# Performance work log

Hardware: AMD Instinct MI355X
Metric: run time of the kernel (lower is better)

## Reference

```python
import jax, jax.numpy as jnp
import numpy as np

ALPHA = 0.5  # distance-decay base (self.alpha)

def setup_inputs() -> dict:
    key = jax.random.key(0)
    N, E, D_IN, D_OUT = 50000, 800000, 128, 128
    k1, k2, k3, k4, k5 = jax.random.split(key, 5)
    h = jax.random.normal(k1, (N, D_IN), dtype=jnp.float32)
    # first N edges are self-loops so every node has in/out degree >= 1
    src = jnp.concatenate([jnp.arange(N), jax.random.randint(k2, (E - N,), 0, N)]).astype(jnp.int32)
    dst = jnp.concatenate([jnp.arange(N), jax.random.randint(k3, (E - N,), 0, N)]).astype(jnp.int32)
    distance = jax.random.randint(k4, (E,), 0, 6).astype(jnp.int32)
    limit = float(np.sqrt(6.0 / (D_IN + D_OUT)))  # xavier_uniform
    weight = jax.random.uniform(k5, (D_IN, D_OUT), jnp.float32, -limit, limit)
    bias = jnp.zeros((D_OUT,), jnp.float32)
    return {"h": h, "src": src, "dst": dst, "distance": distance, "weight": weight, "bias": bias}

def reference(h, src, dst, distance, weight, bias):
    N = h.shape[0]
    ones = jnp.ones(src.shape[0], jnp.float32)
    out_deg = jax.ops.segment_sum(ones, src, num_segments=N)  # [N]
    in_deg = jax.ops.segment_sum(ones, dst, num_segments=N)   # [N]
    # source-side symmetric norm
    feat = h * (out_deg ** -0.5)[:, None]                     # [N, D]
    # per-edge message: gathered src feature * alpha^distance
    w = jnp.power(jnp.float32(ALPHA), distance.astype(jnp.float32))  # [E]
    msg = feat[src] * w[:, None]                              # [E, D]
    # mean over mailbox == segment-sum / in-degree
    agg = jax.ops.segment_sum(msg, dst, num_segments=N) / in_deg[:, None]  # [N, D]
    rst = agg @ weight                                        # [N, D_OUT]
    rst = rst * (in_deg ** -0.5)[:, None] + bias
    return rst
```

## Files before the change

kernel.cpp:

```cpp
#include <hip/hip_runtime.h>


constexpr int D = 128;
constexpr int HC = 32;
constexpr int NWMAX = 25088;
constexpr int PNODES = 32;
constexpr int PCAP = 768;
constexpr int CHUNK = 8192;

typedef __attribute__((ext_vector_type(8))) short bf16x8;
typedef __attribute__((ext_vector_type(4))) float f32x4;

__device__ __forceinline__ float bf16_to_f(unsigned int u16) {
    union { unsigned int u; float f; } c; c.u = u16 << 16; return c.f;
}
__device__ __forceinline__ unsigned int f_to_bf16(float f) {
    union { float f; unsigned int u; } c; c.f = f;
    unsigned int u = c.u;
    u += 0x7fffu + ((u >> 16) & 1u);
    return u >> 16;
}

__global__ __launch_bounds__(256) void k_hist(const int* __restrict__ key,
        unsigned int* __restrict__ slices, int E, int NW, int chunk) {
    __shared__ unsigned int bins[NWMAX];
    for (int i = threadIdx.x; i < NW; i += 256) bins[i] = 0;
    __syncthreads();
    int c = blockIdx.x;
    int e0 = c * chunk, e1 = min(e0 + chunk, E);
    for (int i = e0 + threadIdx.x * 4; i < e1; i += 1024) {
        if (i + 3 < e1) {
            int4 k4 = *(const int4*)&key[i];
            atomicAdd(&bins[k4.x >> 1], 1u << ((k4.x & 1) * 16));
            atomicAdd(&bins[k4.y >> 1], 1u << ((k4.y & 1) * 16));
            atomicAdd(&bins[k4.z >> 1], 1u << ((k4.z & 1) * 16));
            atomicAdd(&bins[k4.w >> 1], 1u << ((k4.w & 1) * 16));
        } else {
            for (int e = i; e < e1; e++)
                atomicAdd(&bins[key[e] >> 1], 1u << ((key[e] & 1) * 16));
        }
    }
    __syncthreads();
    unsigned int* o = slices + (size_t)c * NW;
    for (int i = threadIdx.x; i < NW; i += 256) o[i] = bins[i];
}

__global__ __launch_bounds__(256) void k_scale_cast(const unsigned int* __restrict__ slices,
        const float4* __restrict__ h4, uint4* __restrict__ hs4,
        const float* __restrict__ W, unsigned short* __restrict__ Wt,
        int N, int NW, int wblk) {
    if (blockIdx.x == wblk) {
        for (int i = threadIdx.x; i < D * D; i += 256) {
            int k = i >> 7, n = i & 127;
            Wt[n * D + k] = (unsigned short)f_to_bf16(W[i]);
        }
        return;
    }
    __shared__ float osc[256];
    int n0 = blockIdx.x * 256;
    int n = n0 + threadIdx.x;
    if (n < N) {
        int wi = n >> 1, sh = (n & 1) * 16;
        unsigned int s = 0;
        #pragma unroll 8
        for (int c = 0; c < HC; c++) s += slices[(size_t)c * NW + wi];
        osc[threadIdx.x] = rsqrtf((float)((s >> sh) & 0xffffu));
    }
    __syncthreads();
    int grp = threadIdx.x >> 4, lane = threadIdx.x & 15;
    int rend = min(256, N - n0);
    for (int r = grp; r < rend; r += 16) {
        int row = n0 + r;
        float sc = osc[r];
        float4 a = h4[(size_t)row * 32 + lane * 2];
        float4 b = h4[(size_t)row * 32 + lane * 2 + 1];
        uint4 o;
        o.x = f_to_bf16(a.x * sc) | (f_to_bf16(a.y * sc) << 16);
        o.y = f_to_bf16(a.z * sc) | (f_to_bf16(a.w * sc) << 16);
        o.z = f_to_bf16(b.x * sc) | (f_to_bf16(b.y * sc) << 16);
        o.w = f_to_bf16(b.z * sc) | (f_to_bf16(b.w * sc) << 16);
        hs4[(size_t)row * 16 + lane] = o;
    }
}

__global__ __launch_bounds__(256) void k_partition(const int* __restrict__ src,
        const int* __restrict__ dst, const int* __restrict__ dist,
        int* __restrict__ gcur, unsigned int* __restrict__ gbuf, int E, int P) {
    __shared__ unsigned int sorted[CHUNK];
    __shared__ int gidx[CHUNK];
    extern __shared__ int dyn[];
    int* hist = dyn;
    int* start = dyn + P;
    int* lofs = dyn + 2 * P;
    int* base_g = dyn + 3 * P;
    __shared__ int wsum[4];

    int tid = threadIdx.x;
    int lane = tid & 63, w = tid >> 6;
    int e0 = blockIdx.x * CHUNK;
    int e1 = min(e0 + CHUNK, E);
    int ce = e1 - e0;

    for (int b = tid; b < P; b += 256) hist[b] = 0;
    __syncthreads();

    for (int i = e0 + tid * 4; i < e1; i += 1024) {
        if (i + 3 < e1) {
            int4 d4 = *(const int4*)&dst[i];
            atomicAdd(&hist[d4.x >> 5], 1);
            atomicAdd(&hist[d4.y >> 5], 1);
            atomicAdd(&hist[d4.z >> 5], 1);
            atomicAdd(&hist[d4.w >> 5], 1);
        } else {
            for (int e = i; e < e1; e++) atomicAdd(&hist[dst[e] >> 5], 1);
        }
    }
    __syncthreads();

    int loc[7];
    int s = 0;
    #pragma unroll
    for (int j = 0; j < 7; j++) {
        int b = tid * 7 + j;
        int v = (b < P) ? hist[b] : 0;
        loc[j] = s;
        s += v;
    }
    int x = s;
    #pragma unroll
    for (int off = 1; off < 64; off <<= 1) {
        int t = __shfl_up(x, off, 64);
        if (lane >= off) x += t;
    }
    if (lane == 63) wsum[w] = x;
    __syncthreads();
    int tbase = x - s;
    #pragma unroll
    for (int k = 0; k < 4; k++) if (k < w) tbase += wsum[k];
    #pragma unroll
    for (int j = 0; j < 7; j++) {
        int b = tid * 7 + j;
        if (b < P) {
            int st = tbase + loc[j];
            start[b] = st;
            lofs[b] = st;
            int cnt = hist[b];
            if (cnt) base_g[b] = atomicAdd(&gcur[b], cnt);
        }
    }
    __syncthreads();

    for (int i = e0 + tid * 4; i < e1; i += 1024) {
        if (i + 3 < e1) {
            int4 s4 = *(const int4*)&src[i];
            int4 d4 = *(const int4*)&dst[i];
            int4 q4 = *(const int4*)&dist[i];
            #pragma unroll
            for (int j = 0; j < 4; j++) {
                int sv = (&s4.x)[j], dv = (&d4.x)[j], qv = (&q4.x)[j];
                int p = dv >> 5;
                unsigned int wd = (unsigned)sv | ((unsigned)(dv & 31) << 16)
                                | ((unsigned)qv << 21);
                int pos = atomicAdd(&lofs[p], 1);
                sorted[pos] = wd;
                int rank = base_g[p] + (pos - start[p]);
                gidx[pos] = (rank < PCAP) ? p * PCAP + rank : -1;
            }
        } else {
            for (int e = i; e < e1; e++) {
                int sv = src[e], dv = dst[e], qv = dist[e];
                int p = dv >> 5;
                unsigned int wd = (unsigned)sv | ((unsigned)(dv & 31) << 16)
                                | ((unsigned)qv << 21);
                int pos = atomicAdd(&lofs[p], 1);
                sorted[pos] = wd;
                int rank = base_g[p] + (pos - start[p]);
                gidx[pos] = (rank < PCAP) ? p * PCAP + rank : -1;
            }
        }
    }
    __syncthreads();

    for (int i = tid; i < ce; i += 256) {
        int g = gidx[i];
        if (g >= 0) gbuf[g] = sorted[i];
    }
}

__global__ __launch_bounds__(256, 8) void k_pagg(const uint4* __restrict__ hs4,
        const unsigned int* __restrict__ gbuf, const int* __restrict__ gcur,
        const unsigned short* __restrict__ Wt, const float* __restrict__ bias,
        float* __restrict__ out, int N) {
    __shared__ unsigned int elist[PCAP];
    __shared__ unsigned int slist[PCAP];
    __shared__ int h2[PNODES], st2[PNODES], lo2[PNODES];
    __shared__ unsigned short As[PNODES * 136];
    int p = blockIdx.x;
    int tid = threadIdx.x;
    int cnt = min(gcur[p], PCAP);
    const unsigned int* gp = gbuf + (size_t)p * PCAP;

    if (tid < PNODES) h2[tid] = 0;
    __syncthreads();
    for (int i = tid; i < cnt; i += 256) {
        unsigned int wd = gp[i];
        elist[i] = wd;
        atomicAdd(&h2[(wd >> 16) & 31], 1);
    }
    __syncthreads();
    if (tid < 64) {
        int v = (tid < PNODES) ? h2[tid] : 0;
        int x = v;
        #pragma unroll
        for (int off = 1; off < 32; off <<= 1) {
            int t = __shfl_up(x, off, 64);
            if ((tid & 63) >= off) x += t;
        }
        if (tid < PNODES) { st2[tid] = x - v; lo2[tid] = x - v; }
    }
    __syncthreads();
    for (int i = tid; i < cnt; i += 256) {
        unsigned int wd = elist[i];
        int pos = atomicAdd(&lo2[(wd >> 16) & 31], 1);
        slist[pos] = wd;
    }
    __syncthreads();

    int grp = tid >> 4, lane = tid & 15;
    #pragma unroll
    for (int rep = 0; rep < 2; rep++) {
        int dl = grp * 2 + rep;
        int node = p * PNODES + dl;
        uint4 o = make_uint4(0u, 0u, 0u, 0u);
        if (node < N) {
            int deg = h2[dl];
            int b = st2[dl], e = b + deg;
            float acc[8] = {0.f, 0.f, 0.f, 0.f, 0.f, 0.f, 0.f, 0.f};
            for (int i = b; i < e; i++) {
                unsigned int wd = slist[i];
                int s = wd & 0xffffu;
                float c = __uint_as_float((127u - ((wd >> 21) & 7u)) << 23);
                uint4 hv = hs4[(size_t)s * 16 + lane];
                acc[0] += c * bf16_to_f(hv.x & 0xffffu);
                acc[1] += c * bf16_to_f(hv.x >> 16);
                acc[2] += c * bf16_to_f(hv.y & 0xffffu);
                acc[3] += c * bf16_to_f(hv.y >> 16);
                acc[4] += c * bf16_to_f(hv.z & 0xffffu);
                acc[5] += c * bf16_to_f(hv.z >> 16);
                acc[6] += c * bf16_to_f(hv.w & 0xffffu);
                acc[7] += c * bf16_to_f(hv.w >> 16);
            }
            float fd = (float)deg;
            float sc = rsqrtf(fd) / fd;
            o.x = f_to_bf16(acc[0] * sc) | (f_to_bf16(acc[1] * sc) << 16);
            o.y = f_to_bf16(acc[2] * sc) | (f_to_bf16(acc[3] * sc) << 16);
            o.z = f_to_bf16(acc[4] * sc) | (f_to_bf16(acc[5] * sc) << 16);
            o.w = f_to_bf16(acc[6] * sc) | (f_to_bf16(acc[7] * sc) << 16);
        }
        *(uint4*)&As[dl * 136 + lane * 8] = o;
    }
    __syncthreads();

    int wv = tid >> 6, l64 = tid & 63;
    int m = l64 & 15, quad = l64 >> 4;
    int mt = wv & 1, ntb = (wv >> 1) * 4;
    f32x4 acc2[4];
    #pragma unroll
    for (int t = 0; t < 4; t++) acc2[t] = (f32x4){0.f, 0.f, 0.f, 0.f};
    #pragma unroll
    for (int s = 0; s < 4; s++) {
        bf16x8 a = *(const bf16x8*)&As[(mt * 16 + m) * 136 + quad * 8 + s * 32];
        #pragma unroll
        for (int t = 0; t < 4; t++) {
            int n = (ntb + t) * 16 + m;
            bf16x8 b = *(const bf16x8*)&Wt[n * D + quad * 8 + s * 32];
            acc2[t] = __builtin_amdgcn_mfma_f32_16x16x32_bf16(a, b, acc2[t], 0, 0, 0);
        }
    }
    int orow0 = p * PNODES + mt * 16 + quad * 4;
    #pragma unroll
    for (int t = 0; t < 4; t++) {
        int n = (ntb + t) * 16 + m;
        float bz = bias[n];
        #pragma unroll
        for (int r = 0; r < 4; r++) {
            int grow = orow0 + r;
            if (grow < N) out[(size_t)grow * D + n] = acc2[t][r] + bz;
        }
    }
}

extern "C" void kernel_launch(void* const* d_in, const int* in_sizes, int n_in,
                              void* d_out, int out_size, void* d_ws, size_t ws_size,
                              hipStream_t stream) {
    const float* h    = (const float*)d_in[0];
    const int*   src  = (const int*)d_in[1];
    const int*   dst  = (const int*)d_in[2];
    const int*   dist = (const int*)d_in[3];
    const float* W    = (const float*)d_in[4];
    const float* bias = (const float*)d_in[5];
    float* out = (float*)d_out;
    const int N = in_sizes[0] / D;
    const int E = in_sizes[1];

    const int NW = (N + 1) / 2;
    const int hchunk = (((E + HC - 1) / HC) + 3) & ~3;
    const int P = (N + PNODES - 1) / PNODES;

    char* ws = (char*)d_ws;
    size_t p = 0;
    auto alloc = [&](size_t bytes) -> char* {
        char* r = ws + p;
        p = (p + bytes + 511) & ~(size_t)511;
        return r;
    };
    unsigned int* slices = (unsigned int*)alloc((size_t)HC * NW * 4);
    int* gcur = (int*)alloc((size_t)P * 4);
    unsigned int* gbuf = (unsigned int*)alloc((size_t)P * PCAP * 4);
    unsigned short* hs = (unsigned short*)alloc((size_t)N * D * 2);
    unsigned short* Wt = (unsigned short*)alloc((size_t)D * D * 2);

    hipMemsetAsync(gcur, 0, (size_t)P * 4, stream);
    k_hist<<<HC, 256, 0, stream>>>(src, slices, E, NW, hchunk);
    int nbsc = (N + 255) / 256;
    k_scale_cast<<<nbsc + 1, 256, 0, stream>>>(slices, (const float4*)h, (uint4*)hs,
                                               W, Wt, N, NW, nbsc);
    int nbA = (E + CHUNK - 1) / CHUNK;
    size_t dyn_sz = (size_t)4 * P * 4;
    k_partition<<<nbA, 256, dyn_sz, stream>>>(src, dst, dist, gcur, gbuf, E, P);
    k_pagg<<<P, 256, 0, stream>>>((const uint4*)hs, gbuf, gcur, Wt, bias, out, N);
}
```

Before: 185.0 us.

## Split each node's edge gather across wave sub-groups with batched loads and shuffle reduce

```diff
diff --git a/kernel.cpp b/kernel.cpp
--- a/kernel.cpp
+++ b/kernel.cpp
@@ -2,7 +2,7 @@
 
 
 constexpr int D = 128;
-constexpr int HC = 32;
+constexpr int HC = 64;
 constexpr int NWMAX = 25088;
 constexpr int PNODES = 32;
 constexpr int PCAP = 768;
@@ -187,7 +187,7 @@
     }
 }
 
-__global__ __launch_bounds__(256, 8) void k_pagg(const uint4* __restrict__ hs4,
+__global__ __launch_bounds__(256, 4) void k_pagg(const uint4* __restrict__ hs4,
         const unsigned int* __restrict__ gbuf, const int* __restrict__ gcur,
         const unsigned short* __restrict__ Wt, const float* __restrict__ bias,
         float* __restrict__ out, int N) {
@@ -226,42 +226,59 @@
     }
     __syncthreads();
 
-    int grp = tid >> 4, lane = tid & 15;
-    #pragma unroll
-    for (int rep = 0; rep < 2; rep++) {
-        int dl = grp * 2 + rep;
+    int wv = tid >> 6, l64 = tid & 63;
+    int lane16 = l64 & 15, sub = l64 >> 4;
+    #pragma unroll
+    for (int k = 0; k < 8; k++) {
+        int dl = wv * 8 + k;
         int node = p * PNODES + dl;
-        uint4 o = make_uint4(0u, 0u, 0u, 0u);
-        if (node < N) {
-            int deg = h2[dl];
-            int b = st2[dl], e = b + deg;
-            float acc[8] = {0.f, 0.f, 0.f, 0.f, 0.f, 0.f, 0.f, 0.f};
-            for (int i = b; i < e; i++) {
-                unsigned int wd = slist[i];
-                int s = wd & 0xffffu;
-                float c = __uint_as_float((127u - ((wd >> 21) & 7u)) << 23);
-                uint4 hv = hs4[(size_t)s * 16 + lane];
-                acc[0] += c * bf16_to_f(hv.x & 0xffffu);
-                acc[1] += c * bf16_to_f(hv.x >> 16);
-                acc[2] += c * bf16_to_f(hv.y & 0xffffu);
-                acc[3] += c * bf16_to_f(hv.y >> 16);
-                acc[4] += c * bf16_to_f(hv.z & 0xffffu);
-                acc[5] += c * bf16_to_f(hv.z >> 16);
-                acc[6] += c * bf16_to_f(hv.w & 0xffffu);
-                acc[7] += c * bf16_to_f(hv.w >> 16);
-            }
-            float fd = (float)deg;
-            float sc = rsqrtf(fd) / fd;
-            o.x = f_to_bf16(acc[0] * sc) | (f_to_bf16(acc[1] * sc) << 16);
-            o.y = f_to_bf16(acc[2] * sc) | (f_to_bf16(acc[3] * sc) << 16);
-            o.z = f_to_bf16(acc[4] * sc) | (f_to_bf16(acc[5] * sc) << 16);
-            o.w = f_to_bf16(acc[6] * sc) | (f_to_bf16(acc[7] * sc) << 16);
-        }
-        *(uint4*)&As[dl * 136 + lane * 8] = o;
-    }
-    __syncthreads();
-
-    int wv = tid >> 6, l64 = tid & 63;
+        int deg = h2[dl], b = st2[dl];
+        float acc[8] = {0.f, 0.f, 0.f, 0.f, 0.f, 0.f, 0.f, 0.f};
+        for (int eo = 0; eo < deg; eo += 16) {
+            uint4 hv[4];
+            float cc[4];
+            #pragma unroll
+            for (int j = 0; j < 4; j++) {
+                int off = eo + j * 4 + sub;
+                bool valid = off < deg;
+                unsigned int wd = slist[b + (valid ? off : 0)];
+                cc[j] = valid ? __uint_as_float((127u - ((wd >> 21) & 7u)) << 23)
+                              : 0.f;
+                hv[j] = hs4[(size_t)(wd & 0xffffu) * 16 + lane16];
+            }
+            #pragma unroll
+            for (int j = 0; j < 4; j++) {
+                float c = cc[j];
+                acc[0] += c * bf16_to_f(hv[j].x & 0xffffu);
+                acc[1] += c * bf16_to_f(hv[j].x >> 16);
+                acc[2] += c * bf16_to_f(hv[j].y & 0xffffu);
+                acc[3] += c * bf16_to_f(hv[j].y >> 16);
+                acc[4] += c * bf16_to_f(hv[j].z & 0xffffu);
+                acc[5] += c * bf16_to_f(hv[j].z >> 16);
+                acc[6] += c * bf16_to_f(hv[j].w & 0xffffu);
+                acc[7] += c * bf16_to_f(hv[j].w >> 16);
+            }
+        }
+        #pragma unroll
+        for (int j = 0; j < 8; j++) {
+            acc[j] += __shfl_xor(acc[j], 16, 64);
+            acc[j] += __shfl_xor(acc[j], 32, 64);
+        }
+        if (sub == 0) {
+            uint4 o = make_uint4(0u, 0u, 0u, 0u);
+            if (node < N) {
+                float fd = (float)deg;
+                float sc = rsqrtf(fd) / fd;
+                o.x = f_to_bf16(acc[0] * sc) | (f_to_bf16(acc[1] * sc) << 16);
+                o.y = f_to_bf16(acc[2] * sc) | (f_to_bf16(acc[3] * sc) << 16);
+                o.z = f_to_bf16(acc[4] * sc) | (f_to_bf16(acc[5] * sc) << 16);
+                o.w = f_to_bf16(acc[6] * sc) | (f_to_bf16(acc[7] * sc) << 16);
+            }
+            *(uint4*)&As[dl * 136 + lane16 * 8] = o;
+        }
+    }
+    __syncthreads();
+
     int m = l64 & 15, quad = l64 >> 4;
     int mt = wv & 1, ntb = (wv >> 1) * 4;
     f32x4 acc2[4];
```

Result: faster. 178.5 us (-3.5%).
